# Kernel optimization log

Hardware: AMD Instinct MI355X
Metric: run time of the kernel (lower is better)

Reference implementation:

```python
import jax, jax.numpy as jnp
import numpy as np

N_TRAJS = 8
N_RES = 500
N_BINS = 34
K_CB_DIST = 150.0
FORCE_CUTOFF = 40.0


def setup_inputs() -> dict:
    key = jax.random.key(0)
    k1, k2 = jax.random.split(key)
    # spread coords so pair distances span several bins
    coords_cb = jax.random.normal(k1, (N_TRAJS, N_RES, 3), dtype=jnp.float32) * 8.0
    gaussian_weights = jax.random.uniform(k2, (N_RES, N_RES, N_BINS), dtype=jnp.float32)
    dist_bin_centres = 3.75 + 0.5 * jnp.arange(N_BINS, dtype=jnp.float32)
    sigmas = jnp.full((N_BINS,), 1.25, dtype=jnp.float32)
    return {
        "coords_cb": coords_cb,
        "gaussian_weights": gaussian_weights,
        "dist_bin_centres": dist_bin_centres,
        "sigmas": sigmas,
    }


def reference(coords_cb, gaussian_weights, dist_bin_centres, sigmas):
    # crep[t, i, j] = cb[t, j]; diffs = crep - crep.transpose(1,2) -> cb[j] - cb[i]
    diffs = coords_cb[:, None, :, :] - coords_cb[:, :, None, :]  # [T, i, j, 3]
    dists = jnp.clip(jnp.sqrt(jnp.sum(diffs * diffs, axis=-1)), 0.1, FORCE_CUTOFF)  # [T,i,j]
    norm_diffs = diffs / dists[..., None]
    # per-bin Gaussian mixture energies and radial force
    dfm = dists[..., None] - dist_bin_centres  # [T, i, j, B]
    cb_energies = gaussian_weights[None] * jnp.exp(-0.5 * (dfm / sigmas) ** 2) / sigmas
    forces = jnp.sum(-dfm / (sigmas * sigmas) * cb_energies, axis=-1)  # [T, i, j]
    pair_accs = -forces[..., None] * K_CB_DIST * norm_diffs  # [T, i, j, 3]
    # accs['CB'] += pair_accs.sum(dim=1)
    return jnp.sum(pair_accs, axis=1)  # [T, n_res, 3]
```

## Files before the change

### kernel.cpp

```cpp
#include <hip/hip_runtime.h>

#define NTRAJ 8
#define NRES  500
#define NBINS 34
#define NSLAB NRES
#define OUT_ELEMS (NTRAJ*NRES*3)
#define OUT4 (OUT_ELEMS/4)
#define RED_G   10
#define RED_PER (NSLAB/RED_G)

__global__ __launch_bounds__(256)
void force_main(const float* __restrict__ cb,
                const float* __restrict__ gw,
                const float* __restrict__ cen,
                const float* __restrict__ sig,
                float* __restrict__ part)
{
    const int tid = threadIdx.x;
    const int j   = blockIdx.y * 256 + tid;
    const int i   = blockIdx.x;
    if (j >= NRES) return;

    float cbj[NTRAJ][3];
#pragma unroll
    for (int t = 0; t < NTRAJ; ++t)
#pragma unroll
        for (int c = 0; c < 3; ++c)
            cbj[t][c] = cb[t * (NRES * 3) + j * 3 + c];

    float dx[NTRAJ], dy[NTRAJ], dz[NTRAJ], d[NTRAJ];
#pragma unroll
    for (int t = 0; t < NTRAJ; ++t) {
        const float xi = cb[t * (NRES * 3) + i * 3 + 0];
        const float yi = cb[t * (NRES * 3) + i * 3 + 1];
        const float zi = cb[t * (NRES * 3) + i * 3 + 2];
        dx[t] = cbj[t][0] - xi;
        dy[t] = cbj[t][1] - yi;
        dz[t] = cbj[t][2] - zi;
        float d2 = dx[t] * dx[t] + dy[t] * dy[t] + dz[t] * dz[t];
        float dd = sqrtf(d2);
        d[t] = fminf(fmaxf(dd, 0.1f), 40.0f);
    }

    float force[NTRAJ];
#pragma unroll
    for (int t = 0; t < NTRAJ; ++t) force[t] = 0.0f;

    const float2* g2 = reinterpret_cast<const float2*>(
        gw + (size_t)i * (NRES * NBINS) + (size_t)j * NBINS);

#pragma unroll
    for (int k = 0; k < NBINS / 2; ++k) {
        const float2 wpair = g2[k];
#pragma unroll
        for (int u = 0; u < 2; ++u) {
            const int b   = 2 * k + u;
            const float w = u ? wpair.y : wpair.x;
            const float sv = __builtin_amdgcn_rcpf(sig[b]);
            const float s2 = sv * sv;
            const float c1 = s2 * -0.72134752044448f;
            const float wb = (w * sv) * s2;
            const float cc = cen[b];
#pragma unroll
            for (int t = 0; t < NTRAJ; ++t) {
                const float dfm = d[t] - cc;
                const float e   = __builtin_amdgcn_exp2f((dfm * c1) * dfm);
                force[t] = fmaf(-(dfm * wb), e, force[t]);
            }
        }
    }

    float* p = part + (size_t)i * OUT_ELEMS;
#pragma unroll
    for (int t = 0; t < NTRAJ; ++t) {
        const float s = (force[t] * __builtin_amdgcn_rcpf(d[t])) * -150.0f;
        p[t * (NRES * 3) + j * 3 + 0] = s * dx[t];
        p[t * (NRES * 3) + j * 3 + 1] = s * dy[t];
        p[t * (NRES * 3) + j * 3 + 2] = s * dz[t];
    }
}

__global__ __launch_bounds__(256)
void reduce_k(const float* __restrict__ part, float* __restrict__ out)
{
    const int f = blockIdx.x * 256 + threadIdx.x;
    if (f >= OUT4) return;
    const int g = blockIdx.y;

    const float4* p4 = reinterpret_cast<const float4*>(part);
    float4 s = make_float4(0.f, 0.f, 0.f, 0.f);
#pragma unroll 10
    for (int ic = g * RED_PER; ic < (g + 1) * RED_PER; ++ic) {
        const float4 v = p4[(size_t)ic * OUT4 + f];
        s.x += v.x; s.y += v.y; s.z += v.z; s.w += v.w;
    }
    atomicAdd(out + f * 4 + 0, s.x);
    atomicAdd(out + f * 4 + 1, s.y);
    atomicAdd(out + f * 4 + 2, s.z);
    atomicAdd(out + f * 4 + 3, s.w);
}

extern "C" void kernel_launch(void* const* d_in, const int* in_sizes, int n_in,
                              void* d_out, int out_size, void* d_ws, size_t ws_size,
                              hipStream_t stream)
{
    const float* cb  = (const float*)d_in[0];
    const float* gw  = (const float*)d_in[1];
    const float* cen = (const float*)d_in[2];
    const float* sig = (const float*)d_in[3];
    float* out  = (float*)d_out;
    float* part = (float*)d_ws;

    hipMemsetAsync(out, 0, (size_t)OUT_ELEMS * sizeof(float), stream);

    force_main<<<dim3(NSLAB, 2), 256, 0, stream>>>(cb, gw, cen, sig, part);
    reduce_k<<<dim3((OUT4 + 255) / 256, RED_G), 256, 0, stream>>>(part, out);
}
```

Before: 105.6 us.

## Stage Gaussian weights through LDS and store partials in planar layout

Each block now loads its contiguous slab of gaussian weights with coalesced float2 reads into padded shared memory, instead of every thread doing strided 136-byte-stride reads. Partial forces are written coordinate-planar (t, c, j) so stores are coalesced across j. The reduction kernel maps the planar indices back to the interleaved output layout when doing its atomics. The cost is a __syncthreads, about 36 KB of LDS per block that may limit occupancy, and some extra index arithmetic in the reduction.

Result: slower. 112.5 us (+6.6%).

```diff
diff --git a/kernel.cpp b/kernel.cpp
--- a/kernel.cpp
+++ b/kernel.cpp
@@ -3,11 +3,12 @@
 #define NTRAJ 8
 #define NRES  500
 #define NBINS 34
-#define NSLAB NRES
+#define JT    256
+#define LDSROW 35
 #define OUT_ELEMS (NTRAJ*NRES*3)
 #define OUT4 (OUT_ELEMS/4)
-#define RED_G   10
-#define RED_PER (NSLAB/RED_G)
+#define RED_G 10
+#define RED_PER (NRES/RED_G)
 
 __global__ __launch_bounds__(256)
 void force_main(const float* __restrict__ cb,
@@ -16,17 +17,26 @@
                 const float* __restrict__ sig,
                 float* __restrict__ part)
 {
+    __shared__ float sgw[JT * LDSROW];
     const int tid = threadIdx.x;
-    const int j   = blockIdx.y * 256 + tid;
     const int i   = blockIdx.x;
-    if (j >= NRES) return;
+    const int j0  = blockIdx.y * JT;
+    const int nj  = min(JT, NRES - j0);
 
-    float cbj[NTRAJ][3];
-#pragma unroll
-    for (int t = 0; t < NTRAJ; ++t)
-#pragma unroll
-        for (int c = 0; c < 3; ++c)
-            cbj[t][c] = cb[t * (NRES * 3) + j * 3 + c];
+    const float2* gsrc = reinterpret_cast<const float2*>(
+        gw + (size_t)i * (NRES * NBINS) + (size_t)j0 * NBINS);
+    const int nf2 = nj * (NBINS / 2);
+    for (int f = tid; f < nf2; f += 256) {
+        const float2 v = gsrc[f];
+        const int jj = f / (NBINS / 2);
+        const int bb = f - jj * (NBINS / 2);
+        sgw[jj * LDSROW + 2 * bb + 0] = v.x;
+        sgw[jj * LDSROW + 2 * bb + 1] = v.y;
+    }
+    __syncthreads();
+    if (tid >= nj) return;
+
+    const int j = j0 + tid;
 
     float dx[NTRAJ], dy[NTRAJ], dz[NTRAJ], d[NTRAJ];
 #pragma unroll
@@ -34,28 +44,26 @@
         const float xi = cb[t * (NRES * 3) + i * 3 + 0];
         const float yi = cb[t * (NRES * 3) + i * 3 + 1];
         const float zi = cb[t * (NRES * 3) + i * 3 + 2];
-        dx[t] = cbj[t][0] - xi;
-        dy[t] = cbj[t][1] - yi;
-        dz[t] = cbj[t][2] - zi;
-        float d2 = dx[t] * dx[t] + dy[t] * dy[t] + dz[t] * dz[t];
-        float dd = sqrtf(d2);
-        d[t] = fminf(fmaxf(dd, 0.1f), 40.0f);
+        dx[t] = cb[t * (NRES * 3) + j * 3 + 0] - xi;
+        dy[t] = cb[t * (NRES * 3) + j * 3 + 1] - yi;
+        dz[t] = cb[t * (NRES * 3) + j * 3 + 2] - zi;
+        const float d2 = dx[t] * dx[t] + dy[t] * dy[t] + dz[t] * dz[t];
+        d[t] = fminf(fmaxf(sqrtf(d2), 0.1f), 40.0f);
     }
 
     float force[NTRAJ];
 #pragma unroll
     for (int t = 0; t < NTRAJ; ++t) force[t] = 0.0f;
 
-    const float2* g2 = reinterpret_cast<const float2*>(
-        gw + (size_t)i * (NRES * NBINS) + (size_t)j * NBINS);
-
+    const float* row = &sgw[tid * LDSROW];
 #pragma unroll
     for (int k = 0; k < NBINS / 2; ++k) {
-        const float2 wpair = g2[k];
+        const float w0 = row[2 * k + 0];
+        const float w1 = row[2 * k + 1];
 #pragma unroll
         for (int u = 0; u < 2; ++u) {
             const int b   = 2 * k + u;
-            const float w = u ? wpair.y : wpair.x;
+            const float w = u ? w1 : w0;
             const float sv = __builtin_amdgcn_rcpf(sig[b]);
             const float s2 = sv * sv;
             const float c1 = s2 * -0.72134752044448f;
@@ -74,9 +82,9 @@
 #pragma unroll
     for (int t = 0; t < NTRAJ; ++t) {
         const float s = (force[t] * __builtin_amdgcn_rcpf(d[t])) * -150.0f;
-        p[t * (NRES * 3) + j * 3 + 0] = s * dx[t];
-        p[t * (NRES * 3) + j * 3 + 1] = s * dy[t];
-        p[t * (NRES * 3) + j * 3 + 2] = s * dz[t];
+        p[t * (3 * NRES) + 0 * NRES + j] = s * dx[t];
+        p[t * (3 * NRES) + 1 * NRES + j] = s * dy[t];
+        p[t * (3 * NRES) + 2 * NRES + j] = s * dz[t];
     }
 }
 
@@ -94,10 +102,16 @@
         const float4 v = p4[(size_t)ic * OUT4 + f];
         s.x += v.x; s.y += v.y; s.z += v.z; s.w += v.w;
     }
-    atomicAdd(out + f * 4 + 0, s.x);
-    atomicAdd(out + f * 4 + 1, s.y);
-    atomicAdd(out + f * 4 + 2, s.z);
-    atomicAdd(out + f * 4 + 3, s.w);
+    const int q0 = f * 4;
+    const int t  = q0 / (3 * NRES);
+    const int r  = q0 - t * (3 * NRES);
+    const int c  = r / NRES;
+    const int jj = r - c * NRES;
+    float* o = out + t * (NRES * 3) + jj * 3 + c;
+    atomicAdd(o + 0, s.x);
+    atomicAdd(o + 3, s.y);
+    atomicAdd(o + 6, s.z);
+    atomicAdd(o + 9, s.w);
 }
 
 extern "C" void kernel_launch(void* const* d_in, const int* in_sizes, int n_in,
@@ -113,6 +127,6 @@
 
     hipMemsetAsync(out, 0, (size_t)OUT_ELEMS * sizeof(float), stream);
 
-    force_main<<<dim3(NSLAB, 2), 256, 0, stream>>>(cb, gw, cen, sig, part);
+    force_main<<<dim3(NRES, 2), 256, 0, stream>>>(cb, gw, cen, sig, part);
     reduce_k<<<dim3((OUT4 + 255) / 256, RED_G), 256, 0, stream>>>(part, out);
 }
```
